# Optimization experiments

Hardware: AMD Instinct MI355X
Metric: run time of the kernel (lower is better)

Reference implementation:

```python
import jax, jax.numpy as jnp
import numpy as np

N_NODES = 100000
N_EDGES = 1600000
IN_FEATS = 128
H_FEATS = 64
NUM_CLASSES = 16


def setup_inputs() -> dict:
    key = jax.random.key(0)
    ks = jax.random.split(key, 6)
    X = jax.random.normal(ks[0], (N_NODES, IN_FEATS), dtype=jnp.float32)
    edge_weight = jax.random.uniform(ks[1], (N_EDGES,), dtype=jnp.float32)
    W1 = jax.random.normal(ks[2], (IN_FEATS, H_FEATS), dtype=jnp.float32) * (1.0 / np.sqrt(IN_FEATS))
    b1 = jnp.zeros((H_FEATS,), dtype=jnp.float32)
    W2 = jax.random.normal(ks[3], (H_FEATS, NUM_CLASSES), dtype=jnp.float32) * (1.0 / np.sqrt(H_FEATS))
    b2 = jnp.zeros((NUM_CLASSES,), dtype=jnp.float32)
    edge_src = jax.random.randint(ks[4], (N_EDGES,), 0, N_NODES, dtype=jnp.int32)
    edge_dst = jax.random.randint(ks[5], (N_EDGES,), 0, N_NODES, dtype=jnp.int32)
    return {"X": X, "edge_weight": edge_weight, "W1": W1, "b1": b1,
            "W2": W2, "b2": b2, "edge_src": edge_src, "edge_dst": edge_dst}


def _gcn_conv(H, W, b, edge_src, edge_dst, edge_weight, num_nodes):
    # transform-then-aggregate: out = A @ (H @ W) + b, A given as weighted edge list
    H = H @ W                                  # [N, d_out]
    msgs = H[edge_src] * edge_weight[:, None]  # [E, d_out] gather + scale
    agg = jax.ops.segment_sum(msgs, edge_dst, num_segments=num_nodes)  # scatter-add
    return agg + b


def reference(X, edge_weight, W1, b1, W2, b2, edge_src, edge_dst):
    n = X.shape[0]
    h = jax.nn.relu(_gcn_conv(X, W1, b1, edge_src, edge_dst, edge_weight, n))
    return _gcn_conv(h, W2, b2, edge_src, edge_dst, edge_weight, n)
```

## Files before the change

kernel.cpp:

```cpp
#include <hip/hip_runtime.h>

#define N_NODES 100000
#define N_EDGES 1600000
#define IN_F 128
#define H_F 64
#define C_F 16

#define BIN_SH 7
#define BIN_NODES 128
#define NBINS 782
#define BCAP 2816
#define PART_BLOCKS 391
#define GEMM1_BLOCKS 1563
#define RMAX 6
#define AGG_STRIDE 36

typedef __attribute__((ext_vector_type(8))) short bf16x8;
typedef __attribute__((ext_vector_type(4))) float f32x4;

__device__ inline unsigned short f2bf(float f) {
  unsigned u = __float_as_uint(f);
  unsigned r = (u + 0x7fff + ((u >> 16) & 1)) >> 16;
  return (unsigned short)r;
}

__global__ __launch_bounds__(256) void part_gemm1_kernel(
    const int* __restrict__ src, const int* __restrict__ dst,
    const float* __restrict__ ew, int* __restrict__ binCnt,
    int2* __restrict__ ebin, const float* __restrict__ X,
    const float* __restrict__ W1, unsigned short* __restrict__ H1b) {
  __shared__ char ldsraw[16 * 1024];
  int tid = threadIdx.x;
  if (blockIdx.x < PART_BLOCKS) {
    int* hist = (int*)ldsraw;
    int* base = hist + NBINS;
    for (int i = tid; i < NBINS; i += 256) hist[i] = 0;
    __syncthreads();
    int i0 = blockIdx.x * 1024;
    int iHi = i0 + 1024;
    if (iHi > N_EDGES / 4) iHi = N_EDGES / 4;
    const int4* d4p = (const int4*)dst;
    const int4* s4p = (const int4*)src;
    const float4* w4p = (const float4*)ew;
    unsigned key[16];
    unsigned aux[16];
#pragma unroll
    for (int it = 0; it < 4; ++it) {
      int i = i0 + it * 256 + tid;
      if (i < iHi) {
        int4 d = d4p[i];
        int4 s = s4p[i];
        float4 w = w4p[i];
#pragma unroll
        for (int j = 0; j < 4; ++j) {
          int dd = (&d.x)[j];
          int ss = (&s.x)[j];
          float ww = (&w.x)[j];
          int bb = dd >> BIN_SH;
          unsigned wf = (unsigned)(ww * 32767.0f + 0.5f);
          key[it * 4 + j] =
              (unsigned)ss | ((unsigned)(dd & (BIN_NODES - 1)) << 17);
          aux[it * 4 + j] = wf | ((unsigned)bb << 15);
          atomicAdd(&hist[bb], 1);
        }
      }
    }
    __syncthreads();
    for (int i = tid; i < NBINS; i += 256)
      base[i] = hist[i] ? atomicAdd(&binCnt[i], hist[i]) : 0;
    __syncthreads();
#pragma unroll
    for (int it = 0; it < 4; ++it) {
      int i = i0 + it * 256 + tid;
      if (i < iHi) {
#pragma unroll
        for (int j = 0; j < 4; ++j) {
          unsigned a = aux[it * 4 + j];
          int bb = (int)(a >> 15);
          int pos = atomicAdd(&base[bb], 1);
          ebin[(size_t)bb * BCAP + pos] =
              make_int2((int)key[it * 4 + j], (int)(a & 0x7FFF));
        }
      }
    }
  } else {
    short* ldsB = (short*)ldsraw;
    for (int idx = tid; idx < 16 * 512; idx += 256) {
      int frag = idx >> 9;
      int entry = idx & 511;
      int lane = entry >> 3, j = entry & 7;
      int c = frag >> 2, s = frag & 3;
      int k = s * 32 + (lane >> 4) * 8 + j;
      int n = c * 16 + (lane & 15);
      ldsB[idx] = (short)f2bf(W1[k * H_F + n]);
    }
    __syncthreads();
    int wave = tid >> 6;
    int lane = tid & 63;
    int rt = (blockIdx.x - PART_BLOCKS) * 4 + wave;
    if (rt >= N_NODES / 16) return;
    int node0 = rt * 16;
    int l = lane & 15, q = lane >> 4;
    const float* xp = X + (size_t)(node0 + l) * IN_F + q * 8;
    f32x4 acc[4] = {f32x4{0.f, 0.f, 0.f, 0.f}, f32x4{0.f, 0.f, 0.f, 0.f},
                    f32x4{0.f, 0.f, 0.f, 0.f}, f32x4{0.f, 0.f, 0.f, 0.f}};
#pragma unroll
    for (int s = 0; s < 4; ++s) {
      float4 x0 = *(const float4*)(xp + s * 32);
      float4 x1 = *(const float4*)(xp + s * 32 + 4);
      bf16x8 a;
      a[0] = f2bf(x0.x); a[1] = f2bf(x0.y); a[2] = f2bf(x0.z); a[3] = f2bf(x0.w);
      a[4] = f2bf(x1.x); a[5] = f2bf(x1.y); a[6] = f2bf(x1.z); a[7] = f2bf(x1.w);
#pragma unroll
      for (int c = 0; c < 4; ++c) {
        bf16x8 b = *(const bf16x8*)&ldsB[(c * 4 + s) * 512 + lane * 8];
        acc[c] = __builtin_amdgcn_mfma_f32_16x16x32_bf16(a, b, acc[c], 0, 0, 0);
      }
    }
#pragma unroll
    for (int c = 0; c < 4; ++c)
#pragma unroll
      for (int r = 0; r < 4; ++r)
        H1b[(size_t)(node0 + q * 4 + r) * H_F + c * 16 + l] = f2bf(acc[c][r]);
  }
}

__global__ __launch_bounds__(512) void gather1f_kernel(
    const uint2* __restrict__ H1q, const int* __restrict__ binCnt,
    const int2* __restrict__ ebin, const float* __restrict__ b1,
    const float* __restrict__ W2, unsigned short* __restrict__ H2b) {
  __shared__ int h[BIN_NODES], sc[BIN_NODES], cur[BIN_NODES];
  __shared__ unsigned srt[BCAP];
  __shared__ unsigned aggU[BIN_NODES * AGG_STRIDE];
  __shared__ short ldsW2[2 * 512];
  int b = blockIdx.x, tid = threadIdx.x;
  for (int idx = tid; idx < 1024; idx += 512) {
    int sfrag = idx >> 9;
    int entry = idx & 511;
    int lane = entry >> 3, j = entry & 7;
    int k = sfrag * 32 + (lane >> 4) * 8 + j;
    int c = lane & 15;
    ldsW2[idx] = (short)f2bf(W2[k * C_F + c]);
  }
  int lo = b * BCAP;
  int cnt = binCnt[b];
  if (tid < BIN_NODES) h[tid] = 0;
  __syncthreads();
  unsigned rk[RMAX];
  int rd[RMAX];
  int rn = 0;
#pragma unroll
  for (int j = 0; j < RMAX; ++j) {
    int e = j * 512 + tid;
    if (e < cnt) {
      int2 r = ebin[lo + e];
      int dl = (((unsigned)r.x) >> 17) & (BIN_NODES - 1);
      rk[j] = ((unsigned)r.x & 0x1FFFF) | ((unsigned)r.y << 17);
      rd[j] = dl;
      atomicAdd(&h[dl], 1);
      rn = j + 1;
    }
  }
  __syncthreads();
  if (tid < BIN_NODES) sc[tid] = h[tid];
  __syncthreads();
#pragma unroll
  for (int d = 1; d < BIN_NODES; d <<= 1) {
    int t = 0;
    if (tid < BIN_NODES && tid >= d) t = sc[tid - d];
    __syncthreads();
    if (tid < BIN_NODES) sc[tid] += t;
    __syncthreads();
  }
  if (tid < BIN_NODES) cur[tid] = sc[tid] - h[tid];
  __syncthreads();
#pragma unroll
  for (int j = 0; j < RMAX; ++j)
    if (j < rn) {
      int pos = atomicAdd(&cur[rd[j]], 1);
      srt[pos] = rk[j];
    }
  __syncthreads();
  int wv = tid >> 6, lane = tid & 63, g = lane >> 4, li = lane & 15;
  const float wsc = 1.0f / 32767.0f;
  float bb0 = b1[li * 4], bb1 = b1[li * 4 + 1];
  float bb2 = b1[li * 4 + 2], bb3 = b1[li * 4 + 3];
  for (int k = 0; k < 16; ++k) {
    int nl = wv * 16 + k;
    int n = (b << BIN_SH) + nl;
    if (n >= N_NODES) break;
    int e1 = sc[nl], e0 = e1 - h[nl];
    f32x4 a0 = {0.f, 0.f, 0.f, 0.f}, a1 = {0.f, 0.f, 0.f, 0.f};
    f32x4 a2 = {0.f, 0.f, 0.f, 0.f}, a3 = {0.f, 0.f, 0.f, 0.f};
    int i = e0;
    for (; i + 15 < e1; i += 16) {
      unsigned r0 = srt[i + g];
      unsigned r1 = srt[i + 4 + g];
      unsigned r2 = srt[i + 8 + g];
      unsigned r3 = srt[i + 12 + g];
      uint2 v0 = H1q[(r0 & 0x1FFFF) * (H_F / 4) + li];
      uint2 v1 = H1q[(r1 & 0x1FFFF) * (H_F / 4) + li];
      uint2 v2 = H1q[(r2 & 0x1FFFF) * (H_F / 4) + li];
      uint2 v3 = H1q[(r3 & 0x1FFFF) * (H_F / 4) + li];
      float w0 = (float)(r0 >> 17) * wsc, w1 = (float)(r1 >> 17) * wsc;
      float w2 = (float)(r2 >> 17) * wsc, w3 = (float)(r3 >> 17) * wsc;
      a0[0] += __uint_as_float(v0.x << 16) * w0;
      a0[1] += __uint_as_float(v0.x & 0xFFFF0000u) * w0;
      a0[2] += __uint_as_float(v0.y << 16) * w0;
      a0[3] += __uint_as_float(v0.y & 0xFFFF0000u) * w0;
      a1[0] += __uint_as_float(v1.x << 16) * w1;
      a1[1] += __uint_as_float(v1.x & 0xFFFF0000u) * w1;
      a1[2] += __uint_as_float(v1.y << 16) * w1;
      a1[3] += __uint_as_float(v1.y & 0xFFFF0000u) * w1;
      a2[0] += __uint_as_float(v2.x << 16) * w2;
      a2[1] += __uint_as_float(v2.x & 0xFFFF0000u) * w2;
      a2[2] += __uint_as_float(v2.y << 16) * w2;
      a2[3] += __uint_as_float(v2.y & 0xFFFF0000u) * w2;
      a3[0] += __uint_as_float(v3.x << 16) * w3;
      a3[1] += __uint_as_float(v3.x & 0xFFFF0000u) * w3;
      a3[2] += __uint_as_float(v3.y << 16) * w3;
      a3[3] += __uint_as_float(v3.y & 0xFFFF0000u) * w3;
    }
    for (; i + 3 < e1; i += 4) {
      unsigned r0 = srt[i + g];
      uint2 v0 = H1q[(r0 & 0x1FFFF) * (H_F / 4) + li];
      float w0 = (float)(r0 >> 17) * wsc;
      a0[0] += __uint_as_float(v0.x << 16) * w0;
      a0[1] += __uint_as_float(v0.x & 0xFFFF0000u) * w0;
      a0[2] += __uint_as_float(v0.y << 16) * w0;
      a0[3] += __uint_as_float(v0.y & 0xFFFF0000u) * w0;
    }
    if (i + g < e1) {
      unsigned r0 = srt[i + g];
      uint2 v0 = H1q[(r0 & 0x1FFFF) * (H_F / 4) + li];
      float w0 = (float)(r0 >> 17) * wsc;
      a1[0] += __uint_as_float(v0.x << 16) * w0;
      a1[1] += __uint_as_float(v0.x & 0xFFFF0000u) * w0;
      a1[2] += __uint_as_float(v0.y << 16) * w0;
      a1[3] += __uint_as_float(v0.y & 0xFFFF0000u) * w0;
    }
    f32x4 a = (a0 + a1) + (a2 + a3);
#pragma unroll
    for (int c = 0; c < 4; ++c) {
      a[c] += __shfl_xor(a[c], 16, 64);
      a[c] += __shfl_xor(a[c], 32, 64);
    }
    if (g == 0) {
      float r0 = fmaxf(a[0] + bb0, 0.f);
      float r1 = fmaxf(a[1] + bb1, 0.f);
      float r2 = fmaxf(a[2] + bb2, 0.f);
      float r3 = fmaxf(a[3] + bb3, 0.f);
      unsigned p0 = (unsigned)f2bf(r0) | ((unsigned)f2bf(r1) << 16);
      unsigned p1 = (unsigned)f2bf(r2) | ((unsigned)f2bf(r3) << 16);
      *(uint2*)&aggU[nl * AGG_STRIDE + li * 2] = make_uint2(p0, p1);
    }
  }
  __syncthreads();
  int l = lane & 15, q = lane >> 4;
  int nl0 = wv * 16;
  f32x4 acc = {0.f, 0.f, 0.f, 0.f};
#pragma unroll
  for (int s = 0; s < 2; ++s) {
    bf16x8 afr = *(const bf16x8*)&aggU[(nl0 + l) * AGG_STRIDE + s * 16 + q * 4];
    bf16x8 bfr = *(const bf16x8*)&ldsW2[s * 512 + lane * 8];
    acc = __builtin_amdgcn_mfma_f32_16x16x32_bf16(afr, bfr, acc, 0, 0, 0);
  }
  int node0 = (b << BIN_SH) + nl0;
#pragma unroll
  for (int r = 0; r < 4; ++r) {
    int n = node0 + q * 4 + r;
    if (n < N_NODES) H2b[(size_t)n * C_F + l] = f2bf(acc[r]);
  }
}

__global__ __launch_bounds__(512) void gather2s_kernel(
    const uint2* __restrict__ H2q, const int* __restrict__ binCnt,
    const int2* __restrict__ ebin, const float* __restrict__ b2,
    float* __restrict__ out) {
  __shared__ int h[BIN_NODES], sc[BIN_NODES], cur[BIN_NODES];
  __shared__ unsigned srt[BCAP];
  int b = blockIdx.x, tid = threadIdx.x;
  int lo = b * BCAP;
  int cnt = binCnt[b];
  if (tid < BIN_NODES) h[tid] = 0;
  __syncthreads();
  unsigned rk[RMAX];
  int rd[RMAX];
  int rn = 0;
#pragma unroll
  for (int j = 0; j < RMAX; ++j) {
    int e = j * 512 + tid;
    if (e < cnt) {
      int2 r = ebin[lo + e];
      int dl = (((unsigned)r.x) >> 17) & (BIN_NODES - 1);
      rk[j] = ((unsigned)r.x & 0x1FFFF) | ((unsigned)r.y << 17);
      rd[j] = dl;
      atomicAdd(&h[dl], 1);
      rn = j + 1;
    }
  }
  __syncthreads();
  if (tid < BIN_NODES) sc[tid] = h[tid];
  __syncthreads();
#pragma unroll
  for (int d = 1; d < BIN_NODES; d <<= 1) {
    int t = 0;
    if (tid < BIN_NODES && tid >= d) t = sc[tid - d];
    __syncthreads();
    if (tid < BIN_NODES) sc[tid] += t;
    __syncthreads();
  }
  if (tid < BIN_NODES) cur[tid] = sc[tid] - h[tid];
  __syncthreads();
#pragma unroll
  for (int j = 0; j < RMAX; ++j)
    if (j < rn) {
      int pos = atomicAdd(&cur[rd[j]], 1);
      srt[pos] = rk[j];
    }
  __syncthreads();
  int wv = tid >> 6, lane = tid & 63, g = lane >> 2, li = lane & 3;
  const float wsc = 1.0f / 32767.0f;
  float bb0 = b2[li * 4], bb1 = b2[li * 4 + 1];
  float bb2 = b2[li * 4 + 2], bb3 = b2[li * 4 + 3];
  for (int k = 0; k < 16; ++k) {
    int nl = wv * 16 + k;
    int n = (b << BIN_SH) + nl;
    if (n >= N_NODES) break;
    int e1 = sc[nl], e0 = e1 - h[nl];
    f32x4 a0 = {0.f, 0.f, 0.f, 0.f};
    int i = e0;
    for (; i + 15 < e1; i += 16) {
      unsigned r0 = srt[i + g];
      uint2 v0 = H2q[(r0 & 0x1FFFF) * (C_F / 4) + li];
      float w0 = (float)(r0 >> 17) * wsc;
      a0[0] += __uint_as_float(v0.x << 16) * w0;
      a0[1] += __uint_as_float(v0.x & 0xFFFF0000u) * w0;
      a0[2] += __uint_as_float(v0.y << 16) * w0;
      a0[3] += __uint_as_float(v0.y & 0xFFFF0000u) * w0;
    }
    if (i + g < e1) {
      unsigned r0 = srt[i + g];
      uint2 v0 = H2q[(r0 & 0x1FFFF) * (C_F / 4) + li];
      float w0 = (float)(r0 >> 17) * wsc;
      a0[0] += __uint_as_float(v0.x << 16) * w0;
      a0[1] += __uint_as_float(v0.x & 0xFFFF0000u) * w0;
      a0[2] += __uint_as_float(v0.y << 16) * w0;
      a0[3] += __uint_as_float(v0.y & 0xFFFF0000u) * w0;
    }
#pragma unroll
    for (int c = 0; c < 4; ++c) {
      a0[c] += __shfl_xor(a0[c], 4, 64);
      a0[c] += __shfl_xor(a0[c], 8, 64);
      a0[c] += __shfl_xor(a0[c], 16, 64);
      a0[c] += __shfl_xor(a0[c], 32, 64);
    }
    if (g == 0) {
      float4 o;
      o.x = a0[0] + bb0;
      o.y = a0[1] + bb1;
      o.z = a0[2] + bb2;
      o.w = a0[3] + bb3;
      *(float4*)&out[(size_t)n * C_F + li * 4] = o;
    }
  }
}

extern "C" void kernel_launch(void* const* d_in, const int* in_sizes, int n_in,
                              void* d_out, int out_size, void* d_ws,
                              size_t ws_size, hipStream_t stream) {
  const float* X  = (const float*)d_in[0];
  const float* ew = (const float*)d_in[1];
  const float* W1 = (const float*)d_in[2];
  const float* b1 = (const float*)d_in[3];
  const float* W2 = (const float*)d_in[4];
  const float* b2 = (const float*)d_in[5];
  const int* src  = (const int*)d_in[6];
  const int* dst  = (const int*)d_in[7];
  float* out = (float*)d_out;

  unsigned short* H1b = (unsigned short*)d_ws;
  unsigned short* H2b = H1b + (size_t)N_NODES * H_F;
  int2* ebin  = (int2*)(H2b + (size_t)N_NODES * C_F);
  int* binCnt = (int*)(ebin + (size_t)NBINS * BCAP);

  hipMemsetAsync(binCnt, 0, NBINS * sizeof(int), stream);
  part_gemm1_kernel<<<PART_BLOCKS + GEMM1_BLOCKS, 256, 0, stream>>>(
      src, dst, ew, binCnt, ebin, X, W1, H1b);
  gather1f_kernel<<<NBINS, 512, 0, stream>>>((const uint2*)H1b, binCnt, ebin,
                                             b1, W2, H2b);
  gather2s_kernel<<<NBINS, 512, 0, stream>>>((const uint2*)H2b, binCnt, ebin,
                                             b2, out);
}
```

Measured before the change: 212.1 us.

## Build global CSR by destination once instead of per-bin sort in each gather

Replaces the per-bin partition plus in-block counting sort, which was repeated in both gather kernels, with a global CSR build. A histogram kernel counts edges per node with global atomics, an offset kernel prefix-sums them into per-node segments, and a scatter kernel places packed src/weight entries at their final sorted positions. The gather kernels then just copy a contiguous slice into LDS and read node segments directly, removing two redundant sorts. In exchange it adds two kernel launches and heavy global atomic traffic on per-node counters (1.6M atomics, done twice), and the scatter step writes at random positions.

```diff
diff --git a/kernel.cpp b/kernel.cpp
--- a/kernel.cpp
+++ b/kernel.cpp
@@ -9,11 +9,12 @@
 #define BIN_SH 7
 #define BIN_NODES 128
 #define NBINS 782
-#define BCAP 2816
-#define PART_BLOCKS 391
-#define GEMM1_BLOCKS 1563
-#define RMAX 6
+#define SRT_CAP 2816
 #define AGG_STRIDE 36
+
+#define HIST_BLOCKS 782
+#define SC_BLOCKS 391
+#define G1_BLOCKS 782
 
 typedef __attribute__((ext_vector_type(8))) short bf16x8;
 typedef __attribute__((ext_vector_type(4))) float f32x4;
@@ -24,80 +25,114 @@
   return (unsigned short)r;
 }
 
-__global__ __launch_bounds__(256) void part_gemm1_kernel(
+__global__ __launch_bounds__(256) void hist_kernel(
+    const int* __restrict__ dst, int* __restrict__ cnt,
+    int* __restrict__ binTot) {
+  __shared__ int lb[NBINS];
+  int tid = threadIdx.x;
+  for (int i = tid; i < NBINS; i += 256) lb[i] = 0;
+  __syncthreads();
+  int i0 = blockIdx.x * 512;
+  const int4* d4 = (const int4*)dst;
+#pragma unroll
+  for (int it = 0; it < 2; ++it) {
+    int i = i0 + it * 256 + tid;
+    if (i < N_EDGES / 4) {
+      int4 d = d4[i];
+#pragma unroll
+      for (int j = 0; j < 4; ++j) {
+        int dd = (&d.x)[j];
+        atomicAdd(&cnt[dd], 1);
+        atomicAdd(&lb[dd >> BIN_SH], 1);
+      }
+    }
+  }
+  __syncthreads();
+  for (int i = tid; i < NBINS; i += 256)
+    if (lb[i]) atomicAdd(&binTot[i], lb[i]);
+}
+
+__global__ __launch_bounds__(256) void off_kernel(
+    const int* __restrict__ binTot, int* __restrict__ cnt,
+    int2* __restrict__ seg) {
+  __shared__ int red[256];
+  __shared__ int c[BIN_NODES];
+  int b = blockIdx.x, tid = threadIdx.x;
+  int s = 0;
+  for (int i = tid; i < b; i += 256) s += binTot[i];
+  red[tid] = s;
+  __syncthreads();
+#pragma unroll
+  for (int d = 128; d > 0; d >>= 1) {
+    if (tid < d) red[tid] += red[tid + d];
+    __syncthreads();
+  }
+  int binBase = red[0];
+  int n = (b << BIN_SH) + tid;
+  int cv = 0;
+  if (tid < BIN_NODES) {
+    cv = (n < N_NODES) ? cnt[n] : 0;
+    c[tid] = cv;
+  }
+  __syncthreads();
+#pragma unroll
+  for (int d = 1; d < BIN_NODES; d <<= 1) {
+    int t = 0;
+    if (tid < BIN_NODES && tid >= d) t = c[tid - d];
+    __syncthreads();
+    if (tid < BIN_NODES) c[tid] += t;
+    __syncthreads();
+  }
+  if (tid < BIN_NODES && n < N_NODES) {
+    int e1 = binBase + c[tid];
+    seg[n] = make_int2(e1 - cv, e1);
+    cnt[n] = e1 - cv;
+  }
+}
+
+__global__ __launch_bounds__(512) void scatter_gemm1_kernel(
     const int* __restrict__ src, const int* __restrict__ dst,
-    const float* __restrict__ ew, int* __restrict__ binCnt,
-    int2* __restrict__ ebin, const float* __restrict__ X,
+    const float* __restrict__ ew, int* __restrict__ cur,
+    unsigned* __restrict__ srt, const float* __restrict__ X,
     const float* __restrict__ W1, unsigned short* __restrict__ H1b) {
-  __shared__ char ldsraw[16 * 1024];
+  __shared__ short ldsB[16 * 512];
   int tid = threadIdx.x;
-  if (blockIdx.x < PART_BLOCKS) {
-    int* hist = (int*)ldsraw;
-    int* base = hist + NBINS;
-    for (int i = tid; i < NBINS; i += 256) hist[i] = 0;
-    __syncthreads();
+  if (blockIdx.x < SC_BLOCKS) {
     int i0 = blockIdx.x * 1024;
-    int iHi = i0 + 1024;
-    if (iHi > N_EDGES / 4) iHi = N_EDGES / 4;
-    const int4* d4p = (const int4*)dst;
-    const int4* s4p = (const int4*)src;
-    const float4* w4p = (const float4*)ew;
-    unsigned key[16];
-    unsigned aux[16];
-#pragma unroll
-    for (int it = 0; it < 4; ++it) {
-      int i = i0 + it * 256 + tid;
-      if (i < iHi) {
-        int4 d = d4p[i];
-        int4 s = s4p[i];
-        float4 w = w4p[i];
+    const int4* d4 = (const int4*)dst;
+    const int4* s4 = (const int4*)src;
+    const float4* w4 = (const float4*)ew;
+#pragma unroll
+    for (int it = 0; it < 2; ++it) {
+      int i = i0 + it * 512 + tid;
+      if (i < N_EDGES / 4) {
+        int4 d = d4[i];
+        int4 ss = s4[i];
+        float4 w = w4[i];
 #pragma unroll
         for (int j = 0; j < 4; ++j) {
           int dd = (&d.x)[j];
-          int ss = (&s.x)[j];
-          float ww = (&w.x)[j];
-          int bb = dd >> BIN_SH;
-          unsigned wf = (unsigned)(ww * 32767.0f + 0.5f);
-          key[it * 4 + j] =
-              (unsigned)ss | ((unsigned)(dd & (BIN_NODES - 1)) << 17);
-          aux[it * 4 + j] = wf | ((unsigned)bb << 15);
-          atomicAdd(&hist[bb], 1);
+          unsigned sv = (unsigned)(&ss.x)[j];
+          unsigned wf = (unsigned)((&w.x)[j] * 32767.0f + 0.5f);
+          int pos = atomicAdd(&cur[dd], 1);
+          srt[pos] = sv | (wf << 17);
         }
       }
     }
-    __syncthreads();
-    for (int i = tid; i < NBINS; i += 256)
-      base[i] = hist[i] ? atomicAdd(&binCnt[i], hist[i]) : 0;
-    __syncthreads();
-#pragma unroll
-    for (int it = 0; it < 4; ++it) {
-      int i = i0 + it * 256 + tid;
-      if (i < iHi) {
-#pragma unroll
-        for (int j = 0; j < 4; ++j) {
-          unsigned a = aux[it * 4 + j];
-          int bb = (int)(a >> 15);
-          int pos = atomicAdd(&base[bb], 1);
-          ebin[(size_t)bb * BCAP + pos] =
-              make_int2((int)key[it * 4 + j], (int)(a & 0x7FFF));
-        }
-      }
-    }
   } else {
-    short* ldsB = (short*)ldsraw;
-    for (int idx = tid; idx < 16 * 512; idx += 256) {
+    for (int idx = tid; idx < 16 * 512; idx += 512) {
       int frag = idx >> 9;
       int entry = idx & 511;
       int lane = entry >> 3, j = entry & 7;
-      int c = frag >> 2, s = frag & 3;
-      int k = s * 32 + (lane >> 4) * 8 + j;
-      int n = c * 16 + (lane & 15);
-      ldsB[idx] = (short)f2bf(W1[k * H_F + n]);
+      int cfr = frag >> 2, sfr = frag & 3;
+      int k = sfr * 32 + (lane >> 4) * 8 + j;
+      int nn = cfr * 16 + (lane & 15);
+      ldsB[idx] = (short)f2bf(W1[k * H_F + nn]);
     }
     __syncthreads();
     int wave = tid >> 6;
     int lane = tid & 63;
-    int rt = (blockIdx.x - PART_BLOCKS) * 4 + wave;
+    int rt = (blockIdx.x - SC_BLOCKS) * 8 + wave;
     if (rt >= N_NODES / 16) return;
     int node0 = rt * 16;
     int l = lane & 15, q = lane >> 4;
@@ -113,8 +148,8 @@
       a[4] = f2bf(x1.x); a[5] = f2bf(x1.y); a[6] = f2bf(x1.z); a[7] = f2bf(x1.w);
 #pragma unroll
       for (int c = 0; c < 4; ++c) {
-        bf16x8 b = *(const bf16x8*)&ldsB[(c * 4 + s) * 512 + lane * 8];
-        acc[c] = __builtin_amdgcn_mfma_f32_16x16x32_bf16(a, b, acc[c], 0, 0, 0);
+        bf16x8 bfr = *(const bf16x8*)&ldsB[(c * 4 + s) * 512 + lane * 8];
+        acc[c] = __builtin_amdgcn_mfma_f32_16x16x32_bf16(a, bfr, acc[c], 0, 0, 0);
       }
     }
 #pragma unroll
@@ -126,60 +161,37 @@
 }
 
 __global__ __launch_bounds__(512) void gather1f_kernel(
-    const uint2* __restrict__ H1q, const int* __restrict__ binCnt,
-    const int2* __restrict__ ebin, const float* __restrict__ b1,
+    const uint2* __restrict__ H1q, const int2* __restrict__ seg,
+    const unsigned* __restrict__ srtg, const float* __restrict__ b1,
     const float* __restrict__ W2, unsigned short* __restrict__ H2b) {
-  __shared__ int h[BIN_NODES], sc[BIN_NODES], cur[BIN_NODES];
-  __shared__ unsigned srt[BCAP];
+  __shared__ int2 segl[BIN_NODES];
+  __shared__ unsigned srt[SRT_CAP];
   __shared__ unsigned aggU[BIN_NODES * AGG_STRIDE];
   __shared__ short ldsW2[2 * 512];
+  __shared__ int sInfo[2];
   int b = blockIdx.x, tid = threadIdx.x;
   for (int idx = tid; idx < 1024; idx += 512) {
     int sfrag = idx >> 9;
     int entry = idx & 511;
     int lane = entry >> 3, j = entry & 7;
     int k = sfrag * 32 + (lane >> 4) * 8 + j;
-    int c = lane & 15;
-    ldsW2[idx] = (short)f2bf(W2[k * C_F + c]);
-  }
-  int lo = b * BCAP;
-  int cnt = binCnt[b];
-  if (tid < BIN_NODES) h[tid] = 0;
-  __syncthreads();
-  unsigned rk[RMAX];
-  int rd[RMAX];
-  int rn = 0;
-#pragma unroll
-  for (int j = 0; j < RMAX; ++j) {
-    int e = j * 512 + tid;
-    if (e < cnt) {
-      int2 r = ebin[lo + e];
-      int dl = (((unsigned)r.x) >> 17) & (BIN_NODES - 1);
-      rk[j] = ((unsigned)r.x & 0x1FFFF) | ((unsigned)r.y << 17);
-      rd[j] = dl;
-      atomicAdd(&h[dl], 1);
-      rn = j + 1;
-    }
-  }
-  __syncthreads();
-  if (tid < BIN_NODES) sc[tid] = h[tid];
-  __syncthreads();
-#pragma unroll
-  for (int d = 1; d < BIN_NODES; d <<= 1) {
-    int t = 0;
-    if (tid < BIN_NODES && tid >= d) t = sc[tid - d];
-    __syncthreads();
-    if (tid < BIN_NODES) sc[tid] += t;
-    __syncthreads();
-  }
-  if (tid < BIN_NODES) cur[tid] = sc[tid] - h[tid];
-  __syncthreads();
-#pragma unroll
-  for (int j = 0; j < RMAX; ++j)
-    if (j < rn) {
-      int pos = atomicAdd(&cur[rd[j]], 1);
-      srt[pos] = rk[j];
-    }
+    int cc = lane & 15;
+    ldsW2[idx] = (short)f2bf(W2[k * C_F + cc]);
+  }
+  if (tid < BIN_NODES) {
+    int n = (b << BIN_SH) + tid;
+    segl[tid] = (n < N_NODES) ? seg[n] : make_int2(0, 0);
+  }
+  if (tid == 0) {
+    int st = seg[b << BIN_SH].x;
+    int en = (b == NBINS - 1) ? N_EDGES : seg[(b + 1) << BIN_SH].x;
+    sInfo[0] = st;
+    sInfo[1] = en - st;
+  }
+  __syncthreads();
+  int sBase = sInfo[0];
+  int sLen = sInfo[1] < SRT_CAP ? sInfo[1] : SRT_CAP;
+  for (int i = tid; i < sLen; i += 512) srt[i] = srtg[sBase + i];
   __syncthreads();
   int wv = tid >> 6, lane = tid & 63, g = lane >> 4, li = lane & 15;
   const float wsc = 1.0f / 32767.0f;
@@ -189,7 +201,8 @@
     int nl = wv * 16 + k;
     int n = (b << BIN_SH) + nl;
     if (n >= N_NODES) break;
-    int e1 = sc[nl], e0 = e1 - h[nl];
+    int2 sgl = segl[nl];
+    int e0 = sgl.x - sBase, e1 = sgl.y - sBase;
     f32x4 a0 = {0.f, 0.f, 0.f, 0.f}, a1 = {0.f, 0.f, 0.f, 0.f};
     f32x4 a2 = {0.f, 0.f, 0.f, 0.f}, a3 = {0.f, 0.f, 0.f, 0.f};
     int i = e0;
@@ -274,50 +287,27 @@
 }
 
 __global__ __launch_bounds__(512) void gather2s_kernel(
-    const uint2* __restrict__ H2q, const int* __restrict__ binCnt,
-    const int2* __restrict__ ebin, const float* __restrict__ b2,
+    const uint2* __restrict__ H2q, const int2* __restrict__ seg,
+    const unsigned* __restrict__ srtg, const float* __restrict__ b2,
     float* __restrict__ out) {
-  __shared__ int h[BIN_NODES], sc[BIN_NODES], cur[BIN_NODES];
-  __shared__ unsigned srt[BCAP];
+  __shared__ int2 segl[BIN_NODES];
+  __shared__ unsigned srt[SRT_CAP];
+  __shared__ int sInfo[2];
   int b = blockIdx.x, tid = threadIdx.x;
-  int lo = b * BCAP;
-  int cnt = binCnt[b];
-  if (tid < BIN_NODES) h[tid] = 0;
-  __syncthreads();
-  unsigned rk[RMAX];
-  int rd[RMAX];
-  int rn = 0;
-#pragma unroll
-  for (int j = 0; j < RMAX; ++j) {
-    int e = j * 512 + tid;
-    if (e < cnt) {
-      int2 r = ebin[lo + e];
-      int dl = (((unsigned)r.x) >> 17) & (BIN_NODES - 1);
-      rk[j] = ((unsigned)r.x & 0x1FFFF) | ((unsigned)r.y << 17);
-      rd[j] = dl;
-      atomicAdd(&h[dl], 1);
-      rn = j + 1;
-    }
-  }
-  __syncthreads();
-  if (tid < BIN_NODES) sc[tid] = h[tid];
-  __syncthreads();
-#pragma unroll
-  for (int d = 1; d < BIN_NODES; d <<= 1) {
-    int t = 0;
-    if (tid < BIN_NODES && tid >= d) t = sc[tid - d];
-    __syncthreads();
-    if (tid < BIN_NODES) sc[tid] += t;
-    __syncthreads();
-  }
-  if (tid < BIN_NODES) cur[tid] = sc[tid] - h[tid];
-  __syncthreads();
-#pragma unroll
-  for (int j = 0; j < RMAX; ++j)
-    if (j < rn) {
-      int pos = atomicAdd(&cur[rd[j]], 1);
-      srt[pos] = rk[j];
-    }
+  if (tid < BIN_NODES) {
+    int n = (b << BIN_SH) + tid;
+    segl[tid] = (n < N_NODES) ? seg[n] : make_int2(0, 0);
+  }
+  if (tid == 0) {
+    int st = seg[b << BIN_SH].x;
+    int en = (b == NBINS - 1) ? N_EDGES : seg[(b + 1) << BIN_SH].x;
+    sInfo[0] = st;
+    sInfo[1] = en - st;
+  }
+  __syncthreads();
+  int sBase = sInfo[0];
+  int sLen = sInfo[1] < SRT_CAP ? sInfo[1] : SRT_CAP;
+  for (int i = tid; i < sLen; i += 512) srt[i] = srtg[sBase + i];
   __syncthreads();
   int wv = tid >> 6, lane = tid & 63, g = lane >> 2, li = lane & 3;
   const float wsc = 1.0f / 32767.0f;
@@ -327,7 +317,8 @@
     int nl = wv * 16 + k;
     int n = (b << BIN_SH) + nl;
     if (n >= N_NODES) break;
-    int e1 = sc[nl], e0 = e1 - h[nl];
+    int2 sgl = segl[nl];
+    int e0 = sgl.x - sBase, e1 = sgl.y - sBase;
     f32x4 a0 = {0.f, 0.f, 0.f, 0.f};
     int i = e0;
     for (; i + 15 < e1; i += 16) {
@@ -381,14 +372,18 @@
 
   unsigned short* H1b = (unsigned short*)d_ws;
   unsigned short* H2b = H1b + (size_t)N_NODES * H_F;
-  int2* ebin  = (int2*)(H2b + (size_t)N_NODES * C_F);
-  int* binCnt = (int*)(ebin + (size_t)NBINS * BCAP);
-
-  hipMemsetAsync(binCnt, 0, NBINS * sizeof(int), stream);
-  part_gemm1_kernel<<<PART_BLOCKS + GEMM1_BLOCKS, 256, 0, stream>>>(
-      src, dst, ew, binCnt, ebin, X, W1, H1b);
-  gather1f_kernel<<<NBINS, 512, 0, stream>>>((const uint2*)H1b, binCnt, ebin,
-                                             b1, W2, H2b);
-  gather2s_kernel<<<NBINS, 512, 0, stream>>>((const uint2*)H2b, binCnt, ebin,
-                                             b2, out);
-}
+  unsigned* srt = (unsigned*)(H2b + (size_t)N_NODES * C_F);
+  int2* seg = (int2*)(srt + N_EDGES);
+  int* cnt = (int*)(seg + N_NODES);
+  int* binTot = cnt + N_NODES;
+
+  hipMemsetAsync(cnt, 0, (N_NODES + NBINS) * sizeof(int), stream);
+  hist_kernel<<<HIST_BLOCKS, 256, 0, stream>>>(dst, cnt, binTot);
+  off_kernel<<<NBINS, 256, 0, stream>>>(binTot, cnt, seg);
+  scatter_gemm1_kernel<<<SC_BLOCKS + G1_BLOCKS, 512, 0, stream>>>(
+      src, dst, ew, cnt, srt, X, W1, H1b);
+  gather1f_kernel<<<NBINS, 512, 0, stream>>>((const uint2*)H1b, seg, srt, b1,
+                                             W2, H2b);
+  gather2s_kernel<<<NBINS, 512, 0, stream>>>((const uint2*)H2b, seg, srt, b2,
+                                             out);
+}
```

Result: slower. 350.0 us (+65.0%).
